# Optimization experiments

Measured on AMD Instinct MI355X. Metric: run time of the kernel, lower is better.

## Reference

```python
import jax, jax.numpy as jnp
import numpy as np

CH = 256
K = 8
INNER = CH // K  # 32


def setup_inputs() -> dict:
    key = jax.random.key(0)
    ks = jax.random.split(key, 9)
    B, C, H, W = 4, CH, 64, 64
    s = 0.02
    return {
        "x": jax.random.normal(ks[0], (B, C, H, W), dtype=jnp.float32),
        "wq": jax.random.normal(ks[1], (INNER, C), dtype=jnp.float32) * s,
        "bq": jnp.zeros((INNER,), dtype=jnp.float32),
        "wk": jax.random.normal(ks[2], (INNER, C), dtype=jnp.float32) * s,
        "bk": jnp.zeros((INNER,), dtype=jnp.float32),
        "wv": jax.random.normal(ks[3], (INNER, C), dtype=jnp.float32) * s,
        "bv": jnp.zeros((INNER,), dtype=jnp.float32),
        "wo": jax.random.normal(ks[4], (C, INNER), dtype=jnp.float32) * s,
        "bo": jnp.zeros((C,), dtype=jnp.float32),
    }


def reference(x, wq, bq, wk, bk, wv, bv, wo, bo):
    B, C, H, W = x.shape
    N = H * W
    xf = x.reshape(B, C, N)
    # 1x1 convs == channel matmuls
    q = jnp.einsum("oc,bcn->bon", wq, xf) + bq[None, :, None]  # [B, inner, N]
    k = jnp.einsum("oc,bcn->bon", wk, xf) + bk[None, :, None]
    v = jnp.einsum("oc,bcn->bon", wv, xf) + bv[None, :, None]
    # energy[b,i,j] = <q[:,i], k[:,j]> (unscaled, as in original)
    energy = jnp.einsum("bci,bcj->bij", q, k)  # [B, N, N]
    attn = jax.nn.softmax(energy, axis=-1)
    # out[b,c,i] = sum_j v[b,c,j] * attn[b,i,j]  (bmm with attn^T)
    out = jnp.einsum("bcj,bij->bci", v, attn)  # [B, inner, N]
    out = jnp.einsum("oc,bcn->bon", wo, out) + bo[None, :, None]  # [B, C, N]
    return out.reshape(B, C, H, W)
```

## Files before the change

### kernel.cpp

```cpp
#include <hip/hip_runtime.h>

#define NB 4
#define NC 256
#define NI 32
#define NN 4096
#define NSPLIT 8
#define KVQ (NN / NSPLIT)

typedef short s8v __attribute__((ext_vector_type(8)));
typedef float f4v __attribute__((ext_vector_type(4)));
typedef float f16v __attribute__((ext_vector_type(16)));
typedef unsigned u4v __attribute__((ext_vector_type(4)));

__device__ __forceinline__ unsigned short f2bf(float f) {
  unsigned u = __builtin_bit_cast(unsigned, f);
  return (unsigned short)((u + 0x7FFFu + ((u >> 16) & 1u)) >> 16);
}

__device__ __forceinline__ float fast_exp2(float x) {
  float r;
  asm("v_exp_f32 %0, %1" : "=v"(r) : "v"(x));
  return r;
}

__global__ __launch_bounds__(256) void qkv_proj(
    const float* __restrict__ x,
    const float* __restrict__ wq, const float* __restrict__ bq,
    const float* __restrict__ wk, const float* __restrict__ bk,
    const float* __restrict__ wv, const float* __restrict__ bv,
    unsigned short* __restrict__ Qb, unsigned short* __restrict__ Kb,
    unsigned short* __restrict__ Vt) {
  __shared__ __align__(16) float wl[NI * NC];
  const int tid = threadIdx.x;
  const int proj = blockIdx.x >> 8;
  const int bt = blockIdx.x & 255;
  const int b = bt >> 6;
  const int n = (bt & 63) * 64 + (tid & 63);
  const int ob = (tid >> 6) * 8;

  const float* w = proj == 0 ? wq : (proj == 1 ? wk : wv);
  const float* bias = proj == 0 ? bq : (proj == 1 ? bk : bv);

#pragma unroll
  for (int i = 0; i < 8; ++i)
    *reinterpret_cast<float4*>(&wl[(i * 256 + tid) * 4]) =
        *reinterpret_cast<const float4*>(&w[(i * 256 + tid) * 4]);
  __syncthreads();

  float acc[8] = {};
  const float* xp = x + ((size_t)b * NC) * NN + n;
#pragma unroll 2
  for (int c0 = 0; c0 < NC; c0 += 4) {
    const float xv0 = xp[(size_t)(c0 + 0) * NN];
    const float xv1 = xp[(size_t)(c0 + 1) * NN];
    const float xv2 = xp[(size_t)(c0 + 2) * NN];
    const float xv3 = xp[(size_t)(c0 + 3) * NN];
#pragma unroll
    for (int e = 0; e < 8; ++e) {
      const float4 w4 = *reinterpret_cast<const float4*>(&wl[(ob + e) * NC + c0]);
      acc[e] += w4.x * xv0 + w4.y * xv1 + w4.z * xv2 + w4.w * xv3;
    }
  }

  if (proj < 2) {
    const float sc = proj ? 1.44269504089f : 1.0f;
    s8v pv;
#pragma unroll
    for (int e = 0; e < 8; ++e) pv[e] = (short)f2bf((acc[e] + bias[ob + e]) * sc);
    unsigned short* dst = proj == 0 ? Qb : Kb;
    *reinterpret_cast<s8v*>(&dst[((size_t)b * NN + n) * NI + ob]) = pv;
  } else {
#pragma unroll
    for (int e = 0; e < 8; ++e)
      Vt[((size_t)b * NI + ob + e) * NN + n] = f2bf(acc[e] + bias[ob + e]);
  }
}

__global__ __launch_bounds__(256) void attn_part(
    const unsigned short* __restrict__ Qb, const unsigned short* __restrict__ Kb,
    const unsigned short* __restrict__ Vt,
    unsigned short* __restrict__ Opart, float* __restrict__ Lpart) {
  const int tid = threadIdx.x;
  const int split = blockIdx.x >> 7;
  const int bt = blockIdx.x & 127;
  const int b = bt >> 5;
  const int qw = ((bt & 31) << 7) + ((tid >> 6) << 5);
  const int lane = tid & 63;
  const int l31 = lane & 31;
  const int hi = lane >> 5;

  const unsigned short* qp = Qb + ((size_t)b * NN + qw + l31) * NI + 8 * hi;
  const s8v qf0 = *reinterpret_cast<const s8v*>(qp);
  const s8v qf1 = *reinterpret_cast<const s8v*>(qp + 16);

  const unsigned short* kp = Kb + ((size_t)b * NN + (size_t)split * KVQ + l31) * NI + 8 * hi;
  const unsigned short* vp = Vt + ((size_t)b * NI + l31) * NN + (size_t)split * KVQ + 8 * hi;

  const f16v zero16 = {};
  f16v oacc = {};
  float lsum = 0.f;

#pragma unroll 2
  for (int kv = 0; kv < KVQ; kv += 32) {
    const s8v kf0 = *reinterpret_cast<const s8v*>(kp + (size_t)kv * NI);
    const s8v kf1 = *reinterpret_cast<const s8v*>(kp + (size_t)kv * NI + 16);
    const s8v vf0 = *reinterpret_cast<const s8v*>(vp + kv);
    const s8v vf1 = *reinterpret_cast<const s8v*>(vp + kv + 16);

    f16v S = __builtin_amdgcn_mfma_f32_32x32x16_bf16(kf0, qf0, zero16, 0, 0, 0);
    S = __builtin_amdgcn_mfma_f32_32x32x16_bf16(kf1, qf1, S, 0, 0, 0);

    float p[16];
#pragma unroll
    for (int r = 0; r < 16; ++r) p[r] = fast_exp2(S[r]);
    float t0 = (p[0] + p[1]) + (p[2] + p[3]);
    float t1 = (p[4] + p[5]) + (p[6] + p[7]);
    float t2 = (p[8] + p[9]) + (p[10] + p[11]);
    float t3 = (p[12] + p[13]) + (p[14] + p[15]);
    lsum += (t0 + t1) + (t2 + t3);

    unsigned d[8];
#pragma unroll
    for (int j = 0; j < 8; ++j)
      asm("v_cvt_pk_bf16_f32 %0, %1, %2" : "=v"(d[j]) : "v"(p[2 * j]), "v"(p[2 * j + 1]));
    asm("v_permlane32_swap_b32 %0, %1" : "+v"(d[0]), "+v"(d[2]));
    asm("v_permlane32_swap_b32 %0, %1" : "+v"(d[1]), "+v"(d[3]));
    asm("v_permlane32_swap_b32 %0, %1" : "+v"(d[4]), "+v"(d[6]));
    asm("v_permlane32_swap_b32 %0, %1" : "+v"(d[5]), "+v"(d[7]));

    const u4v a0 = {d[0], d[1], d[2], d[3]};
    const u4v a1 = {d[4], d[5], d[6], d[7]};
    const s8v pa0 = __builtin_bit_cast(s8v, a0);
    const s8v pa1 = __builtin_bit_cast(s8v, a1);

    oacc = __builtin_amdgcn_mfma_f32_32x32x16_bf16(pa0, vf0, oacc, 0, 0, 0);
    oacc = __builtin_amdgcn_mfma_f32_32x32x16_bf16(pa1, vf1, oacc, 0, 0, 0);
  }

  lsum += __shfl_xor(lsum, 32, 64);

  unsigned short* op = Opart + (((size_t)split * NB + b) * NN + qw) * NI + l31;
#pragma unroll
  for (int r = 0; r < 16; ++r) {
    const int qr = (r & 3) + 8 * (r >> 2) + 4 * hi;
    op[(size_t)qr * NI] = f2bf(oacc[r]);
  }
  if (hi == 0)
    Lpart[((size_t)split * NB + b) * NN + qw + l31] = lsum;
}

__global__ __launch_bounds__(256) void combine_proj(
    const unsigned short* __restrict__ Opart, const float* __restrict__ Lpart,
    const float* __restrict__ wo, const float* __restrict__ bo,
    float* __restrict__ out) {
  __shared__ __align__(16) float o_lds[NI][65];
  __shared__ float linv[64];
  const int tid = threadIdx.x;
  const int g2 = blockIdx.x >> 8;
  const int bt = blockIdx.x & 255;
  const int b = bt >> 6;
  const int q0 = (bt & 63) * 64;

  {
    const int qs = tid >> 2, cg = tid & 3;
    float s[8] = {};
#pragma unroll
    for (int sp = 0; sp < NSPLIT; ++sp) {
      const s8v v = *reinterpret_cast<const s8v*>(
          &Opart[(((size_t)sp * NB + b) * NN + q0 + qs) * NI + cg * 8]);
#pragma unroll
      for (int e = 0; e < 8; ++e) {
        const unsigned u = (unsigned)(unsigned short)v[e];
        s[e] += __builtin_bit_cast(float, u << 16);
      }
    }
#pragma unroll
    for (int e = 0; e < 8; ++e) o_lds[cg * 8 + e][qs] = s[e];
  }
  if (tid < 64) {
    float l = 0.f;
#pragma unroll
    for (int sp = 0; sp < NSPLIT; ++sp)
      l += Lpart[((size_t)sp * NB + b) * NN + q0 + tid];
    linv[tid] = 1.0f / l;
  }
  __syncthreads();

  const int q = tid & 63;
  const float il = linv[q];
  float xv[NI];
#pragma unroll
  for (int c = 0; c < NI; ++c) xv[c] = o_lds[c][q] * il;

  float* op2 = out + ((size_t)b * NC) * NN + q0 + q;
  const int co0 = g2 * 64 + (tid >> 6) * 16;
#pragma unroll
  for (int cc = 0; cc < 16; ++cc) {
    const int co = co0 + cc;
    float a = bo[co];
#pragma unroll
    for (int c4 = 0; c4 < 8; ++c4) {
      const float4 w4 = *reinterpret_cast<const float4*>(&wo[co * NI + c4 * 4]);
      a += w4.x * xv[c4 * 4] + w4.y * xv[c4 * 4 + 1] +
           w4.z * xv[c4 * 4 + 2] + w4.w * xv[c4 * 4 + 3];
    }
    op2[(size_t)co * NN] = a;
  }
}

extern "C" void kernel_launch(void* const* d_in, const int* in_sizes, int n_in,
                              void* d_out, int out_size, void* d_ws, size_t ws_size,
                              hipStream_t stream) {
  const float* x  = (const float*)d_in[0];
  const float* wq = (const float*)d_in[1];
  const float* bq = (const float*)d_in[2];
  const float* wk = (const float*)d_in[3];
  const float* bk = (const float*)d_in[4];
  const float* wv = (const float*)d_in[5];
  const float* bv = (const float*)d_in[6];
  const float* wo = (const float*)d_in[7];
  const float* bo = (const float*)d_in[8];
  float* out = (float*)d_out;

  unsigned short* Qb = (unsigned short*)d_ws;
  unsigned short* Kb = Qb + (size_t)NB * NN * NI;
  unsigned short* Vt = Kb + (size_t)NB * NN * NI;
  unsigned short* Opart = Vt + (size_t)NB * NI * NN;
  float* Lpart = (float*)(Opart + (size_t)NSPLIT * NB * NN * NI);

  qkv_proj<<<3 * NB * (NN / 64), 256, 0, stream>>>(x, wq, bq, wk, bk, wv, bv, Qb, Kb, Vt);
  attn_part<<<NSPLIT * NB * (NN / 128), 256, 0, stream>>>(Qb, Kb, Vt, Opart, Lpart);
  combine_proj<<<4 * NB * (NN / 64), 256, 0, stream>>>(Opart, Lpart, wo, bo, out);
}
```

Before: 147.9 us.

## Split projection kernels across more blocks and read weights via scalar loads

The QKV projection stops staging the full weight matrix in LDS. Each block now computes 4 output channels per wave, reading weights through wave-uniform (readfirstlane) addresses, and the grid is doubled. The output projection grid is also doubled so each thread handles 8 output channels instead of 16, and the attention inner loop unroll goes from 2 to 4. This is meant to raise occupancy and parallelism and to drop the LDS fill and barrier, at the cost of reading x twice as often across the projection blocks.

```diff
diff --git a/kernel.cpp b/kernel.cpp
--- a/kernel.cpp
+++ b/kernel.cpp
@@ -7,8 +7,8 @@
 #define NSPLIT 8
 #define KVQ (NN / NSPLIT)
 
+typedef short s4v __attribute__((ext_vector_type(4)));
 typedef short s8v __attribute__((ext_vector_type(8)));
-typedef float f4v __attribute__((ext_vector_type(4)));
 typedef float f16v __attribute__((ext_vector_type(16)));
 typedef unsigned u4v __attribute__((ext_vector_type(4)));
 
@@ -30,49 +30,48 @@
     const float* __restrict__ wv, const float* __restrict__ bv,
     unsigned short* __restrict__ Qb, unsigned short* __restrict__ Kb,
     unsigned short* __restrict__ Vt) {
-  __shared__ __align__(16) float wl[NI * NC];
   const int tid = threadIdx.x;
-  const int proj = blockIdx.x >> 8;
+  const int ph = blockIdx.x >> 8;
+  const int proj = ph >> 1;
+  const int half = ph & 1;
   const int bt = blockIdx.x & 255;
   const int b = bt >> 6;
   const int n = (bt & 63) * 64 + (tid & 63);
-  const int ob = (tid >> 6) * 8;
-
-  const float* w = proj == 0 ? wq : (proj == 1 ? wk : wv);
-  const float* bias = proj == 0 ? bq : (proj == 1 ? bk : bv);
-
-#pragma unroll
-  for (int i = 0; i < 8; ++i)
-    *reinterpret_cast<float4*>(&wl[(i * 256 + tid) * 4]) =
-        *reinterpret_cast<const float4*>(&w[(i * 256 + tid) * 4]);
-  __syncthreads();
-
-  float acc[8] = {};
+  const int obu = __builtin_amdgcn_readfirstlane(half * 16 + (tid >> 6) * 4);
+
+  const float* w;
+  const float* bias;
+  if (proj == 0) { w = wq; bias = bq; }
+  else if (proj == 1) { w = wk; bias = bk; }
+  else { w = wv; bias = bv; }
+  const float* wp = w + (size_t)obu * NC;
+
+  float acc[4] = {};
   const float* xp = x + ((size_t)b * NC) * NN + n;
-#pragma unroll 2
+#pragma unroll 4
   for (int c0 = 0; c0 < NC; c0 += 4) {
     const float xv0 = xp[(size_t)(c0 + 0) * NN];
     const float xv1 = xp[(size_t)(c0 + 1) * NN];
     const float xv2 = xp[(size_t)(c0 + 2) * NN];
     const float xv3 = xp[(size_t)(c0 + 3) * NN];
 #pragma unroll
-    for (int e = 0; e < 8; ++e) {
-      const float4 w4 = *reinterpret_cast<const float4*>(&wl[(ob + e) * NC + c0]);
+    for (int e = 0; e < 4; ++e) {
+      const float4 w4 = *reinterpret_cast<const float4*>(&wp[e * NC + c0]);
       acc[e] += w4.x * xv0 + w4.y * xv1 + w4.z * xv2 + w4.w * xv3;
     }
   }
 
   if (proj < 2) {
     const float sc = proj ? 1.44269504089f : 1.0f;
-    s8v pv;
-#pragma unroll
-    for (int e = 0; e < 8; ++e) pv[e] = (short)f2bf((acc[e] + bias[ob + e]) * sc);
+    s4v pv;
+#pragma unroll
+    for (int e = 0; e < 4; ++e) pv[e] = (short)f2bf((acc[e] + bias[obu + e]) * sc);
     unsigned short* dst = proj == 0 ? Qb : Kb;
-    *reinterpret_cast<s8v*>(&dst[((size_t)b * NN + n) * NI + ob]) = pv;
+    *reinterpret_cast<s4v*>(&dst[((size_t)b * NN + n) * NI + obu]) = pv;
   } else {
 #pragma unroll
-    for (int e = 0; e < 8; ++e)
-      Vt[((size_t)b * NI + ob + e) * NN + n] = f2bf(acc[e] + bias[ob + e]);
+    for (int e = 0; e < 4; ++e)
+      Vt[((size_t)b * NI + obu + e) * NN + n] = f2bf(acc[e] + bias[obu + e]);
   }
 }
 
@@ -100,7 +99,7 @@
   f16v oacc = {};
   float lsum = 0.f;
 
-#pragma unroll 2
+#pragma unroll 4
   for (int kv = 0; kv < KVQ; kv += 32) {
     const s8v kf0 = *reinterpret_cast<const s8v*>(kp + (size_t)kv * NI);
     const s8v kf1 = *reinterpret_cast<const s8v*>(kp + (size_t)kv * NI + 16);
@@ -193,9 +192,9 @@
   for (int c = 0; c < NI; ++c) xv[c] = o_lds[c][q] * il;
 
   float* op2 = out + ((size_t)b * NC) * NN + q0 + q;
-  const int co0 = g2 * 64 + (tid >> 6) * 16;
-#pragma unroll
-  for (int cc = 0; cc < 16; ++cc) {
+  const int co0 = g2 * 32 + (tid >> 6) * 8;
+#pragma unroll
+  for (int cc = 0; cc < 8; ++cc) {
     const int co = co0 + cc;
     float a = bo[co];
 #pragma unroll
@@ -228,7 +227,7 @@
   unsigned short* Opart = Vt + (size_t)NB * NI * NN;
   float* Lpart = (float*)(Opart + (size_t)NSPLIT * NB * NN * NI);
 
-  qkv_proj<<<3 * NB * (NN / 64), 256, 0, stream>>>(x, wq, bq, wk, bk, wv, bv, Qb, Kb, Vt);
+  qkv_proj<<<3 * 2 * NB * (NN / 64), 256, 0, stream>>>(x, wq, bq, wk, bk, wv, bv, Qb, Kb, Vt);
   attn_part<<<NSPLIT * NB * (NN / 128), 256, 0, stream>>>(Qb, Kb, Vt, Opart, Lpart);
-  combine_proj<<<4 * NB * (NN / 64), 256, 0, stream>>>(Opart, Lpart, wo, bo, out);
-}
+  combine_proj<<<8 * NB * (NN / 64), 256, 0, stream>>>(Opart, Lpart, wo, bo, out);
+}
```

Result: no change. 149.5 us (+1.1%).
